# Kernel tuning notes

Hardware: AMD Instinct MI355X
Metric: run time of the kernel (lower is better)

Reference implementation:

```python
import jax, jax.numpy as jnp
import numpy as np
from jax import lax

PADDING_L = 30  # causal: kernel_size - 1


def setup_inputs() -> dict:
    key = jax.random.key(0)
    k1, k2 = jax.random.split(key)
    T, B, C = 4096, 8, 1024
    H, K = 16, 31
    x = jax.random.normal(k1, (T, B, C), dtype=jnp.float32)
    weight = jax.random.normal(k2, (H, K), dtype=jnp.float32)
    return {"x": x, "weight": weight}


def reference(x, weight):
    # x: [T, B, C]; weight: [H, K]
    T, B, C = x.shape
    H, K = weight.shape
    R = C // H  # channels per head share the same kernel
    # weight_softmax=True: normalize kernel taps per head
    w = jax.nn.softmax(weight, axis=-1)            # [H, K]
    wc = jnp.repeat(w, R, axis=0)[:, None, :]      # [C, 1, K] depthwise kernel
    xb = jnp.transpose(x, (1, 2, 0))               # [B, C, T]
    # lightconv_cuda: out[b,c,t] = sum_k w[h(c),k] * x_pad[b,c,t+k],
    # left pad = padding_l, right pad = K-1-padding_l (cross-correlation)
    out = lax.conv_general_dilated(
        xb, wc,
        window_strides=(1,),
        padding=[(PADDING_L, K - 1 - PADDING_L)],
        feature_group_count=C,
        dimension_numbers=("NCH", "OIH", "NCH"),
    )                                              # [B, C, T]
    return jnp.transpose(out, (2, 0, 1))           # [T, B, C]
```

## Files before the change

kernel.cpp:

```cpp
#include <hip/hip_runtime.h>
#include <math.h>

#define T_DIM 4096
#define B_DIM 8
#define C_DIM 1024
#define H_DIM 16
#define K_DIM 31
#define PAD_L 30
#define HALO 30
#define TILE_T 16
#define WROWS (TILE_T + HALO)
#define BLOCK 256
#define CC 256

typedef __attribute__((ext_vector_type(4))) float f32x4;

__device__ __forceinline__ void stage16(const float* g, float* l) {
    __builtin_amdgcn_global_load_lds(
        (const __attribute__((address_space(1))) void*)g,
        (__attribute__((address_space(3))) void*)l,
        16, 0, 0);
}

template <int J>
__device__ __forceinline__ void conv_all(const float* col,
                                         const float (&taps)[K_DIM],
                                         float (&acc)[TILE_T],
                                         float* po, long stride) {
    if constexpr (J < WROWS) {
        const float xj = col[J * CC];
        constexpr int ilo = (J > HALO) ? (J - HALO) : 0;
        constexpr int ihi = (J < TILE_T - 1) ? J : TILE_T - 1;
        #pragma unroll
        for (int i = ilo; i <= ihi; ++i) {
            if (i == J) acc[i] = taps[0] * xj;
            else        acc[i] = fmaf(taps[J - i], xj, acc[i]);
        }
        if constexpr (J >= HALO)
            po[(long)(J - HALO) * stride] = acc[J - HALO];
        conv_all<J + 1>(col, taps, acc, po, stride);
    }
}

__global__ __launch_bounds__(BLOCK, 3) void lightconv_kernel(
    const float* __restrict__ x,
    const float* __restrict__ w,
    float* __restrict__ out)
{
    __shared__ float tile[WROWS][CC];

    const int tid    = threadIdx.x;
    const int lane   = tid & 63;
    const int wv     = tid >> 6;
    const int colBlk = blockIdx.x;
    const int tBlk   = blockIdx.y;
    const int t0     = tBlk * TILE_T;
    const int cc0    = colBlk * CC;
    const long stride = (long)B_DIM * C_DIM;

    {
        const int r0 = wv * 12;
        const int rn = (wv == 3) ? WROWS - 36 : 12;
        const float* gbase = x + (long)(t0 - HALO) * stride + cc0 + lane * 4;
        #pragma unroll
        for (int i = 0; i < 12; ++i) {
            if (i < rn) {
                const int r = r0 + i;
                if (t0 - HALO + r >= 0) {
                    stage16(gbase + (long)r * stride, &tile[r][0]);
                } else {
                    *(f32x4*)&tile[r][lane * 4] = (f32x4){0.f, 0.f, 0.f, 0.f};
                }
            }
        }
    }

    float taps[K_DIM];
    {
        const float* wr = w + (((colBlk & 3) << 2) + wv) * K_DIM;
        float tv[K_DIM];
        float m = -1e30f;
        #pragma unroll
        for (int k = 0; k < K_DIM; ++k) { tv[k] = wr[k]; m = fmaxf(m, tv[k]); }
        float s = 0.f;
        #pragma unroll
        for (int k = 0; k < K_DIM; ++k) { tv[k] = __expf(tv[k] - m); s += tv[k]; }
        const float inv = 1.0f / s;
        #pragma unroll
        for (int k = 0; k < K_DIM; ++k)
            taps[k] = __int_as_float(__builtin_amdgcn_readfirstlane(
                          __float_as_int(tv[k] * inv)));
    }

    __syncthreads();

    float acc[TILE_T];
    float* po = out + (long)t0 * stride + cc0 + tid;
    conv_all<0>(&tile[0][0] + tid, taps, acc, po, stride);
}

extern "C" void kernel_launch(void* const* d_in, const int* in_sizes, int n_in,
                              void* d_out, int out_size, void* d_ws, size_t ws_size,
                              hipStream_t stream) {
    const float* x = (const float*)d_in[0];
    const float* w = (const float*)d_in[1];
    float* out = (float*)d_out;

    dim3 grid((B_DIM * C_DIM) / CC, T_DIM / TILE_T);
    lightconv_kernel<<<grid, BLOCK, 0, stream>>>(x, w, out);
}
```

Before: 230.8 us.

## Replace LDS-tiled conv with register-streaming sliding-window accumulator over long time segments

Drops the shared-memory tile with its 30-row halo. Each thread now streams its own column through a 128-step time segment, keeping a 32-entry rotating accumulator ring and an 8-deep register prefetch queue for input rows. This removes LDS staging, the block barrier and most of the halo re-read overhead, since the halo is now 31 of 128 rows instead of 30 of 16. A warm-up pass rebuilds the accumulators from the preceding 31 rows. The costs are much higher register pressure and fewer blocks for latency hiding.

After: 244.2 us. 1.06x slower.

```diff
diff --git a/kernel.cpp b/kernel.cpp
--- a/kernel.cpp
+++ b/kernel.cpp
@@ -6,76 +6,62 @@
 #define C_DIM 1024
 #define H_DIM 16
 #define K_DIM 31
-#define PAD_L 30
-#define HALO 30
-#define TILE_T 16
-#define WROWS (TILE_T + HALO)
+#define NT 32
+#define L_SEG 128
 #define BLOCK 256
-#define CC 256
+#define DP 8
+#define STRIDE (B_DIM * C_DIM)
 
-typedef __attribute__((ext_vector_type(4))) float f32x4;
 
-__device__ __forceinline__ void stage16(const float* g, float* l) {
-    __builtin_amdgcn_global_load_lds(
-        (const __attribute__((address_space(1))) void*)g,
-        (__attribute__((address_space(3))) void*)l,
-        16, 0, 0);
-}
-
-template <int J>
-__device__ __forceinline__ void conv_all(const float* col,
-                                         const float (&taps)[K_DIM],
-                                         float (&acc)[TILE_T],
-                                         float* po, long stride) {
-    if constexpr (J < WROWS) {
-        const float xj = col[J * CC];
-        constexpr int ilo = (J > HALO) ? (J - HALO) : 0;
-        constexpr int ihi = (J < TILE_T - 1) ? J : TILE_T - 1;
+template <int M>
+__device__ __forceinline__ void warm(const float* pw,
+                                     float (&xr)[DP],
+                                     const float (&tp)[NT],
+                                     float (&acc)[NT]) {
+    if constexpr (M < 31) {
+        const float v = xr[(M + 1) & 7];
         #pragma unroll
-        for (int i = ilo; i <= ihi; ++i) {
-            if (i == J) acc[i] = taps[0] * xj;
-            else        acc[i] = fmaf(taps[J - i], xj, acc[i]);
+        for (int j = 1; j <= 30; ++j) {
+            if (j >= 31 - M)
+                acc[(M + 1 + j) & 31] = fmaf(tp[31 - j], v, acc[(M + 1 + j) & 31]);
         }
-        if constexpr (J >= HALO)
-            po[(long)(J - HALO) * stride] = acc[J - HALO];
-        conv_all<J + 1>(col, taps, acc, po, stride);
+        xr[(M + 1) & 7] = pw[(long)(M + DP) * STRIDE];
+        warm<M + 1>(pw, xr, tp, acc);
     }
 }
 
-__global__ __launch_bounds__(BLOCK, 3) void lightconv_kernel(
+template <int SB, bool LAST>
+__device__ __forceinline__ void bstep(const float* pin,
+                                      float* pout,
+                                      float (&xr)[DP],
+                                      const float (&tp)[NT],
+                                      float (&acc)[NT]) {
+    if constexpr (SB < 32) {
+        const float v = xr[SB & 7];
+        pout[(long)SB * STRIDE] = fmaf(tp[31], v, acc[SB]);
+        #pragma unroll
+        for (int j = 1; j <= 30; ++j)
+            acc[(SB + j) & 31] = fmaf(tp[31 - j], v, acc[(SB + j) & 31]);
+        acc[(SB + 31) & 31] = 0.0f;
+        if constexpr (!LAST || SB < 24)
+            xr[SB & 7] = pin[(long)(SB + DP) * STRIDE];
+        bstep<SB + 1, LAST>(pin, pout, xr, tp, acc);
+    }
+}
+
+__global__ __launch_bounds__(BLOCK, 4) void lightconv_kernel(
     const float* __restrict__ x,
     const float* __restrict__ w,
     float* __restrict__ out)
 {
-    __shared__ float tile[WROWS][CC];
-
     const int tid    = threadIdx.x;
-    const int lane   = tid & 63;
     const int wv     = tid >> 6;
     const int colBlk = blockIdx.x;
-    const int tBlk   = blockIdx.y;
-    const int t0     = tBlk * TILE_T;
-    const int cc0    = colBlk * CC;
-    const long stride = (long)B_DIM * C_DIM;
+    const int tseg   = blockIdx.y;
+    const int cc     = colBlk * BLOCK + tid;
+    const long t0    = (long)tseg * L_SEG;
 
-    {
-        const int r0 = wv * 12;
-        const int rn = (wv == 3) ? WROWS - 36 : 12;
-        const float* gbase = x + (long)(t0 - HALO) * stride + cc0 + lane * 4;
-        #pragma unroll
-        for (int i = 0; i < 12; ++i) {
-            if (i < rn) {
-                const int r = r0 + i;
-                if (t0 - HALO + r >= 0) {
-                    stage16(gbase + (long)r * stride, &tile[r][0]);
-                } else {
-                    *(f32x4*)&tile[r][lane * 4] = (f32x4){0.f, 0.f, 0.f, 0.f};
-                }
-            }
-        }
-    }
-
-    float taps[K_DIM];
+    float tp[NT];
     {
         const float* wr = w + (((colBlk & 3) << 2) + wv) * K_DIM;
         float tv[K_DIM];
@@ -86,17 +72,39 @@
         #pragma unroll
         for (int k = 0; k < K_DIM; ++k) { tv[k] = __expf(tv[k] - m); s += tv[k]; }
         const float inv = 1.0f / s;
+        tp[0] = 0.0f;
         #pragma unroll
         for (int k = 0; k < K_DIM; ++k)
-            taps[k] = __int_as_float(__builtin_amdgcn_readfirstlane(
-                          __float_as_int(tv[k] * inv)));
+            tp[k + 1] = __int_as_float(__builtin_amdgcn_readfirstlane(
+                            __float_as_int(tv[k] * inv)));
     }
 
-    __syncthreads();
+    float acc[NT];
+    #pragma unroll
+    for (int i = 0; i < NT; ++i) acc[i] = 0.0f;
 
-    float acc[TILE_T];
-    float* po = out + (long)t0 * stride + cc0 + tid;
-    conv_all<0>(&tile[0][0] + tid, taps, acc, po, stride);
+    float xr[DP];
+    if (tseg > 0) {
+        const float* pw = x + (t0 - 31) * STRIDE + cc;
+        #pragma unroll
+        for (int m = 0; m < DP; ++m)
+            xr[(m + 1) & 7] = pw[(long)m * STRIDE];
+        warm<0>(pw, xr, tp, acc);
+    } else {
+        #pragma unroll
+        for (int m = 0; m < DP; ++m)
+            xr[m] = x[(long)m * STRIDE + cc];
+    }
+
+    const float* pin = x   + t0 * STRIDE + cc;
+    float*       pout = out + t0 * STRIDE + cc;
+    #pragma unroll 1
+    for (int b = 0; b < 3; ++b) {
+        bstep<0, false>(pin, pout, xr, tp, acc);
+        pin  += 32 * STRIDE;
+        pout += 32 * STRIDE;
+    }
+    bstep<0, true>(pin, pout, xr, tp, acc);
 }
 
 extern "C" void kernel_launch(void* const* d_in, const int* in_sizes, int n_in,
@@ -106,6 +114,6 @@
     const float* w = (const float*)d_in[1];
     float* out = (float*)d_out;
 
-    dim3 grid((B_DIM * C_DIM) / CC, T_DIM / TILE_T);
+    dim3 grid((B_DIM * C_DIM) / BLOCK, T_DIM / L_SEG);
     lightconv_kernel<<<grid, BLOCK, 0, stream>>>(x, w, out);
 }
```
